# Optimization experiments

Measured on AMD Instinct MI355X. Metric: run time of the kernel, lower is better.

Reference implementation:

```python
import jax, jax.numpy as jnp
import numpy as np

B, L = 16, 512          # samples x tokens-per-sample
S = B * L               # total packed tokens
H, HKV, D = 16, 4, 128  # query heads, kv heads, head_dim
G = H // HKV            # GQA group size
HID = 2048
EPS = 1e-6


def rmsnorm(x, w):
    # Qwen2RMSNorm: fp32 variance, scale by weight
    v = jnp.mean(x.astype(jnp.float32) ** 2, axis=-1, keepdims=True)
    return (x.astype(jnp.float32) * jax.lax.rsqrt(v + EPS)).astype(x.dtype) * w


def rotate_half(x):
    x1, x2 = jnp.split(x, 2, axis=-1)
    return jnp.concatenate([-x2, x1], axis=-1)


def setup_inputs() -> dict:
    key = jax.random.key(0)
    ks = jax.random.split(key, 24)
    f = lambda k, shp, s=0.02: (jax.random.normal(k, shp, dtype=jnp.float32) * s)
    inp = {
        'packed_sequence_und': f(ks[0], (S // 2, HID), 1.0),
        'packed_sequence_gen': f(ks[1], (S // 2, HID), 1.0),
        # und tokens on even slots, gen on odd slots -> irregular scatter
        'packed_und_token_indexes': jnp.arange(0, S, 2, dtype=jnp.int32),
        'packed_gen_token_indexes': jnp.arange(1, S, 2, dtype=jnp.int32),
        # und-path projections (q/k/v have bias, o does not)
        'q_w': f(ks[2], (H * D, HID)), 'q_b': f(ks[3], (H * D,)),
        'k_w': f(ks[4], (HKV * D, HID)), 'k_b': f(ks[5], (HKV * D,)),
        'v_w': f(ks[6], (HKV * D, HID)), 'v_b': f(ks[7], (HKV * D,)),
        'o_w': f(ks[8], (HID, H * D)),
        # gen-path (moe_gen) projections
        'q_w_g': f(ks[9], (H * D, HID)), 'q_b_g': f(ks[10], (H * D,)),
        'k_w_g': f(ks[11], (HKV * D, HID)), 'k_b_g': f(ks[12], (HKV * D,)),
        'v_w_g': f(ks[13], (HKV * D, HID)), 'v_b_g': f(ks[14], (HKV * D,)),
        'o_w_g': f(ks[15], (HID, H * D)),
        # qk-norm weights
        'qn_w': jnp.ones((D,), jnp.float32), 'kn_w': jnp.ones((D,), jnp.float32),
        'qn_w_g': jnp.ones((D,), jnp.float32), 'kn_w_g': jnp.ones((D,), jnp.float32),
    }
    # RoPE cos/sin for packed positions (position resets per sample)
    pos = jnp.tile(jnp.arange(L, dtype=jnp.float32), B)            # [S]
    inv_freq = 1.0 / (1e6 ** (jnp.arange(0, D, 2, dtype=jnp.float32) / D))
    freqs = pos[:, None] * inv_freq[None, :]                       # [S, D/2]
    emb = jnp.concatenate([freqs, freqs], axis=-1)                 # [S, D]
    inp['packed_cos'] = jnp.cos(emb)
    inp['packed_sin'] = jnp.sin(emb)
    return inp


def reference(packed_sequence_und, packed_sequence_gen, packed_cos, packed_sin,
              packed_und_token_indexes, packed_gen_token_indexes,
              q_w, q_b, k_w, k_b, v_w, v_b, o_w,
              q_w_g, q_b_g, k_w_g, k_b_g, v_w_g, v_b_g, o_w_g,
              qn_w, kn_w, qn_w_g, kn_w_g):
    ui, gi = packed_und_token_indexes, packed_gen_token_indexes
    # dual-path QKV projection + index scatter into shared packed buffers
    q = jnp.zeros((S, H * D), jnp.float32)
    q = q.at[ui].set(packed_sequence_und @ q_w.T + q_b)
    q = q.at[gi].set(packed_sequence_gen @ q_w_g.T + q_b_g)
    k = jnp.zeros((S, HKV * D), jnp.float32)
    k = k.at[ui].set(packed_sequence_und @ k_w.T + k_b)
    k = k.at[gi].set(packed_sequence_gen @ k_w_g.T + k_b_g)
    v = jnp.zeros((S, HKV * D), jnp.float32)
    v = v.at[ui].set(packed_sequence_und @ v_w.T + v_b)
    v = v.at[gi].set(packed_sequence_gen @ v_w_g.T + v_b_g)

    q = q.reshape(S, H, D)
    k = k.reshape(S, HKV, D)
    v = v.reshape(S, HKV, D)

    # per-stream QK RMSNorm, scattered back
    q = jnp.zeros_like(q).at[ui].set(rmsnorm(q[ui], qn_w)).at[gi].set(rmsnorm(q[gi], qn_w_g))
    k = jnp.zeros_like(k).at[ui].set(rmsnorm(k[ui], kn_w)).at[gi].set(rmsnorm(k[gi], kn_w_g))

    # RoPE (unsqueeze_dim=1)
    cos, sin = packed_cos[:, None, :], packed_sin[:, None, :]
    q = q * cos + rotate_half(q) * sin
    k = k * cos + rotate_half(k) * sin

    # block-diagonal causal attention over packed samples (GQA)
    qb_ = q.reshape(B, L, HKV, G, D)
    kb_ = k.reshape(B, L, HKV, D)
    vb_ = v.reshape(B, L, HKV, D)
    scale = 1.0 / np.sqrt(D)
    scores = jnp.einsum('bqhgd,bkhd->bhgqk', qb_, kb_) * scale   # [B,HKV,G,L,L]
    causal = jnp.tril(jnp.ones((L, L), bool))
    scores = jnp.where(causal, scores, -jnp.inf)
    probs = jax.nn.softmax(scores, axis=-1)
    out = jnp.einsum('bhgqk,bkhd->bqhgd', probs, vb_)            # [B,L,HKV,G,D]
    out = out.reshape(S, H * D)

    out_und = out[ui] @ o_w.T
    out_gen = out[gi] @ o_w_g.T
    return (out_und, out_gen)
```

## Files before the change

kernel.cpp:

```cpp
#include <hip/hip_runtime.h>

typedef __bf16 bf16;
typedef __bf16 bf16x8 __attribute__((ext_vector_type(8)));
typedef float  f32x4  __attribute__((ext_vector_type(4)));

#define HALF   4096
#define S_TOT  8192
#define HID    2048
#define NH     16
#define NKV    4
#define DH     128
#define LSEQ   512

typedef const __attribute__((address_space(1))) void* as1_cvp;
typedef __attribute__((address_space(3))) void* as3_vp;

__device__ __forceinline__ void gl2lds16(const void* g, void* l) {
    __builtin_amdgcn_global_load_lds((as1_cvp)g, (as3_vp)l, 16, 0, 0);
}

__global__ void k_convert(const float* __restrict__ src, bf16* __restrict__ dst, int n4) {
    int i = blockIdx.x * 256 + threadIdx.x;
    if (i >= n4) return;
    float4 v = ((const float4*)src)[i];
    union { bf16 b[4]; ushort4 u; } t;
    t.b[0] = (bf16)v.x; t.b[1] = (bf16)v.y; t.b[2] = (bf16)v.z; t.b[3] = (bf16)v.w;
    ((ushort4*)dst)[i] = t.u;
}

__global__ void k_invtyp(const int* __restrict__ ui, const int* __restrict__ gi,
                         int* __restrict__ it) {
    int t = blockIdx.x * 256 + threadIdx.x;
    if (t < HALF) { it[ui[t]] = t << 1; it[gi[t]] = (t << 1) | 1; }
}

__global__ __launch_bounds__(256) void k_gemm_qkv(
    const bf16* __restrict__ Xu, const bf16* __restrict__ Xg,
    const bf16* __restrict__ Wu, const bf16* __restrict__ Wg,
    const float* __restrict__ qbu, const float* __restrict__ kbu, const float* __restrict__ vbu,
    const float* __restrict__ qbg, const float* __restrict__ kbg, const float* __restrict__ vbg,
    const int* __restrict__ ui, const int* __restrict__ gi,
    bf16* __restrict__ qo, bf16* __restrict__ ko, bf16* __restrict__ vo)
{
    const int gen = blockIdx.z;
    const bf16* X = gen ? Xg : Xu;
    const bf16* W = gen ? Wg : Wu;
    const float* qb = gen ? qbg : qbu;
    const float* kb = gen ? kbg : kbu;
    const float* vb = gen ? vbg : vbu;
    const int* idx = gen ? gi : ui;

    __shared__ __align__(16) bf16 sA[128*32];
    __shared__ __align__(16) bf16 sB[128*32];

    const int tid = threadIdx.x;
    const int wave = tid >> 6, lane = tid & 63;
    const int lm = lane & 15, kq = lane >> 4;
    const int wm = wave >> 1, wn = wave & 1;
    const int m0 = blockIdx.y * 128, n0 = blockIdx.x * 128;

    f32x4 acc[4][4] = {};

    for (int k0 = 0; k0 < HID; k0 += 32) {
        __syncthreads();
        #pragma unroll
        for (int i = 0; i < 2; ++i) {
            const int g = i*4 + wave;
            const int c = g*64 + lane;
            const int row = c >> 2, col = c & 3;
            gl2lds16(X + (size_t)(m0+row)*HID + k0 + col*8, (char*)sA + (size_t)g*1024);
            gl2lds16(W + (size_t)(n0+row)*HID + k0 + col*8, (char*)sB + (size_t)g*1024);
        }
        __syncthreads();
        bf16x8 a[4], b[4];
        #pragma unroll
        for (int i = 0; i < 4; ++i) a[i] = *(const bf16x8*)&sA[(wm*64 + i*16 + lm)*32 + kq*8];
        #pragma unroll
        for (int j = 0; j < 4; ++j) b[j] = *(const bf16x8*)&sB[(wn*64 + j*16 + lm)*32 + kq*8];
        #pragma unroll
        for (int i = 0; i < 4; ++i)
            #pragma unroll
            for (int j = 0; j < 4; ++j)
                acc[i][j] = __builtin_amdgcn_mfma_f32_16x16x32_bf16(a[i], b[j], acc[i][j], 0, 0, 0);
    }

    #pragma unroll
    for (int i = 0; i < 4; ++i) {
        int srow[4];
        #pragma unroll
        for (int r = 0; r < 4; ++r) srow[r] = idx[m0 + wm*64 + i*16 + kq*4 + r];
        #pragma unroll
        for (int j = 0; j < 4; ++j) {
            const int o = n0 + wn*64 + j*16 + lm;
            bf16* dst; float bias; int off0, ld;
            if (o < 2048)      { dst = qo; ld = 2048; off0 = o;        bias = qb[o]; }
            else if (o < 2560) { dst = ko; ld = 512;  off0 = o - 2048; bias = kb[o-2048]; }
            else               { dst = vo; ld = 512;  off0 = o - 2560; bias = vb[o-2560]; }
            #pragma unroll
            for (int r = 0; r < 4; ++r)
                dst[(size_t)srow[r]*ld + off0] = (bf16)(acc[i][j][r] + bias);
        }
    }
}

__global__ __launch_bounds__(256) void k_norm_rope(
    bf16* __restrict__ qbuf, bf16* __restrict__ kbuf,
    const float* __restrict__ cosb, const float* __restrict__ sinb,
    const int* __restrict__ invtyp,
    const float* __restrict__ qnu, const float* __restrict__ qng,
    const float* __restrict__ knu, const float* __restrict__ kng)
{
    const int row = blockIdx.x * 4 + (threadIdx.x >> 6);
    const int lane = threadIdx.x & 63;
    const int s = row / (NH + NKV), hh = row % (NH + NKV);
    const int isg = invtyp[s] & 1;
    bf16* ptr; const float* w;
    if (hh < NH) { ptr = qbuf + (size_t)s*HID + hh*DH;           w = isg ? qng : qnu; }
    else         { ptr = kbuf + (size_t)s*(NKV*DH) + (hh-NH)*DH; w = isg ? kng : knu; }

    const unsigned u = *(const unsigned*)((const unsigned short*)ptr + 2*lane);
    const float f0 = __uint_as_float(u << 16);
    const float f1 = __uint_as_float(u & 0xffff0000u);
    float ss = f0*f0 + f1*f1;
    #pragma unroll
    for (int m = 32; m; m >>= 1) ss += __shfl_xor(ss, m, 64);
    const float r = rsqrtf(ss * (1.0f/128.0f) + 1e-6f);
    const float2 wv = *(const float2*)(w + 2*lane);
    const float xn0 = f0 * r * wv.x;
    const float xn1 = f1 * r * wv.y;
    const float po0 = __shfl_xor(xn0, 32, 64);
    const float po1 = __shfl_xor(xn1, 32, 64);
    const float2 c2 = *(const float2*)(cosb + (size_t)s*DH + 2*lane);
    const float2 s2 = *(const float2*)(sinb + (size_t)s*DH + 2*lane);
    const float sg = (lane < 32) ? -1.0f : 1.0f;
    const float o0 = xn0 * c2.x + sg * po0 * s2.x;
    const float o1 = xn1 * c2.y + sg * po1 * s2.y;
    union { unsigned short us[2]; unsigned u; } t;
    bf16 b0 = (bf16)o0, b1 = (bf16)o1;
    t.us[0] = *(unsigned short*)&b0; t.us[1] = *(unsigned short*)&b1;
    *(unsigned*)((unsigned short*)ptr + 2*lane) = t.u;
}

__global__ __launch_bounds__(256) void k_vtrans(const bf16* __restrict__ v, bf16* __restrict__ vt)
{
    __shared__ __align__(16) bf16 sT[64 * 132];
    const int kvh = blockIdx.y;
    const int s0 = blockIdx.x * 64;
    const int b = s0 >> 9;
    const int pos0 = s0 & 511;
    const int tid = threadIdx.x;

    #pragma unroll
    for (int i = 0; i < 4; ++i) {
        const int c = i*256 + tid;
        const int rowi = c >> 4, col8 = c & 15;
        const uint4 d = *(const uint4*)(v + (size_t)(s0 + rowi)*(NKV*DH) + kvh*DH + col8*8);
        uint2* lp = (uint2*)&sT[rowi*132 + col8*8];
        lp[0] = make_uint2(d.x, d.y);
        lp[1] = make_uint2(d.z, d.w);
    }
    __syncthreads();
    const int dd = tid >> 1, half = tid & 1;
    __align__(16) bf16 tmp[32];
    #pragma unroll
    for (int p = 0; p < 32; ++p) tmp[p] = sT[(half*32 + p)*132 + dd];
    bf16* dst = vt + ((size_t)(b*NKV + kvh)*DH + dd)*LSEQ + pos0 + half*32;
    #pragma unroll
    for (int q = 0; q < 8; ++q) ((ushort4*)dst)[q] = ((ushort4*)tmp)[q];
}

__global__ __launch_bounds__(256) void k_attn(
    const bf16* __restrict__ qbuf, const bf16* __restrict__ kbuf,
    const bf16* __restrict__ vt, const int* __restrict__ invtyp,
    bf16* __restrict__ aop_u, bf16* __restrict__ aop_g)
{
    __shared__ __align__(16) bf16 sQ[64*128];
    __shared__ __align__(16) bf16 sK[64*128];
    __shared__ __align__(16) bf16 sV[128*64];
    __shared__ __align__(16) bf16 sP[4][16*72];

    const int qt = 7 - blockIdx.x;
    const int h = blockIdx.y, b = blockIdx.z;
    const int kvh = h >> 2;
    const int tid = threadIdx.x, wave = tid >> 6, lane = tid & 63;
    const int lm = lane & 15, kq = lane >> 4;
    const int q0 = qt * 64;

    {
        const bf16* qp = qbuf + ((size_t)(b*LSEQ + q0))*HID + h*DH;
        #pragma unroll
        for (int i = 0; i < 4; ++i) {
            const int g = i*4 + wave;
            const int ch = g*64 + lane;
            const int row = ch >> 4, cp = ch & 15;
            const int c = (cp & 8) | ((cp ^ row) & 7);
            gl2lds16(qp + (size_t)row*HID + c*8, (char*)sQ + (size_t)g*1024);
        }
    }

    f32x4 accO[8] = {};
    float mrow[4], lrow[4];
    #pragma unroll
    for (int r = 0; r < 4; ++r) { mrow[r] = -1e30f; lrow[r] = 0.f; }

    const float scale = 0.08838834764831845f;
    bf16* const sPw = &sP[wave][0];

    for (int kt = 0; kt <= qt; ++kt) {
        __syncthreads();
        {
            const bf16* kp = kbuf + ((size_t)(b*LSEQ + kt*64))*(NKV*DH) + kvh*DH;
            const bf16* vp = vt + ((size_t)(b*NKV + kvh)*DH)*LSEQ + kt*64;
            #pragma unroll
            for (int i = 0; i < 4; ++i) {
                const int g = i*4 + wave;
                const int ch = g*64 + lane;
                { const int row = ch >> 4, cp = ch & 15;
                  const int c = (cp & 8) | ((cp ^ row) & 7);
                  gl2lds16(kp + (size_t)row*(NKV*DH) + c*8, (char*)sK + (size_t)g*1024); }
                { const int d = ch >> 3, cp = ch & 7;
                  const int c = (cp ^ d) & 7;
                  gl2lds16(vp + (size_t)d*LSEQ + c*8, (char*)sV + (size_t)g*1024); }
            }
        }
        __syncthreads();

        f32x4 s4[4] = {};
        #pragma unroll
        for (int ks = 0; ks < 4; ++ks) {
            const int cq = ks*4 + kq;
            const int cs = (cq & 8) | ((cq ^ lm) & 7);
            bf16x8 a = *(const bf16x8*)&sQ[(wave*16 + lm)*128 + cs*8];
            #pragma unroll
            for (int nt = 0; nt < 4; ++nt) {
                bf16x8 bk = *(const bf16x8*)&sK[(nt*16 + lm)*128 + cs*8];
                s4[nt] = __builtin_amdgcn_mfma_f32_16x16x32_bf16(a, bk, s4[nt], 0, 0, 0);
            }
        }

        const bool diag = (kt == qt);
        #pragma unroll
        for (int r = 0; r < 4; ++r) {
            const int rloc = wave*16 + kq*4 + r;
            float v0 = s4[0][r], v1 = s4[1][r], v2 = s4[2][r], v3 = s4[3][r];
            if (diag) {
                if (lm      > rloc) v0 = -1e30f;
                if (lm + 16 > rloc) v1 = -1e30f;
                if (lm + 32 > rloc) v2 = -1e30f;
                if (lm + 48 > rloc) v3 = -1e30f;
            }
            float m = fmaxf(fmaxf(v0, v1), fmaxf(v2, v3));
            m = fmaxf(m, __shfl_xor(m, 1, 64));
            m = fmaxf(m, __shfl_xor(m, 2, 64));
            m = fmaxf(m, __shfl_xor(m, 4, 64));
            m = fmaxf(m, __shfl_xor(m, 8, 64));
            const float mnew = fmaxf(mrow[r], m);
            const float p0 = __expf((v0 - mnew) * scale);
            const float p1 = __expf((v1 - mnew) * scale);
            const float p2 = __expf((v2 - mnew) * scale);
            const float p3 = __expf((v3 - mnew) * scale);
            float rs = (p0 + p1) + (p2 + p3);
            rs += __shfl_xor(rs, 1, 64);
            rs += __shfl_xor(rs, 2, 64);
            rs += __shfl_xor(rs, 4, 64);
            rs += __shfl_xor(rs, 8, 64);
            const float alpha = __expf((mrow[r] - mnew) * scale);
            lrow[r] = lrow[r] * alpha + rs;
            mrow[r] = mnew;
            #pragma unroll
            for (int dt = 0; dt < 8; ++dt) accO[dt][r] *= alpha;
            const int prow = (kq*4 + r) * 72;
            sPw[prow + lm]      = (bf16)p0;
            sPw[prow + 16 + lm] = (bf16)p1;
            sPw[prow + 32 + lm] = (bf16)p2;
            sPw[prow + 48 + lm] = (bf16)p3;
        }

        #pragma unroll
        for (int pc = 0; pc < 2; ++pc) {
            bf16x8 ap = *(const bf16x8*)&sPw[lm*72 + pc*32 + kq*8];
            #pragma unroll
            for (int dt = 0; dt < 8; ++dt) {
                const int cv = (pc*4 + kq);
                const int cs = (cv ^ lm) & 7;
                bf16x8 bv = *(const bf16x8*)&sV[(dt*16 + lm)*64 + cs*8];
                accO[dt] = __builtin_amdgcn_mfma_f32_16x16x32_bf16(ap, bv, accO[dt], 0, 0, 0);
            }
        }
    }

    #pragma unroll
    for (int r = 0; r < 4; ++r) {
        const int srow = b*LSEQ + q0 + wave*16 + kq*4 + r;
        const int code = invtyp[srow];
        bf16* dst = (code & 1) ? aop_g : aop_u;
        const size_t off = (size_t)(code >> 1)*HID + h*DH;
        const float inv_l = 1.0f / lrow[r];
        #pragma unroll
        for (int dt = 0; dt < 8; ++dt)
            dst[off + dt*16 + lm] = (bf16)(accO[dt][r] * inv_l);
    }
}

__global__ __launch_bounds__(256) void k_gemm_out(
    const bf16* __restrict__ Au, const bf16* __restrict__ Ag,
    const bf16* __restrict__ Wu, const bf16* __restrict__ Wg,
    float* __restrict__ out)
{
    const int gen = blockIdx.z;
    const bf16* A = gen ? Ag : Au;
    const bf16* W = gen ? Wg : Wu;
    float* O = out + (size_t)gen * HALF * HID;

    __shared__ __align__(16) bf16 sA[128*32];
    __shared__ __align__(16) bf16 sB[128*32];

    const int tid = threadIdx.x;
    const int wave = tid >> 6, lane = tid & 63;
    const int lm = lane & 15, kq = lane >> 4;
    const int wm = wave >> 1, wn = wave & 1;
    const int m0 = blockIdx.y * 128, n0 = blockIdx.x * 128;

    f32x4 acc[4][4] = {};

    for (int k0 = 0; k0 < HID; k0 += 32) {
        __syncthreads();
        #pragma unroll
        for (int i = 0; i < 2; ++i) {
            const int g = i*4 + wave;
            const int c = g*64 + lane;
            const int row = c >> 2, col = c & 3;
            gl2lds16(A + (size_t)(m0+row)*HID + k0 + col*8, (char*)sA + (size_t)g*1024);
            gl2lds16(W + (size_t)(n0+row)*HID + k0 + col*8, (char*)sB + (size_t)g*1024);
        }
        __syncthreads();
        bf16x8 a[4], b[4];
        #pragma unroll
        for (int i = 0; i < 4; ++i) a[i] = *(const bf16x8*)&sA[(wm*64 + i*16 + lm)*32 + kq*8];
        #pragma unroll
        for (int j = 0; j < 4; ++j) b[j] = *(const bf16x8*)&sB[(wn*64 + j*16 + lm)*32 + kq*8];
        #pragma unroll
        for (int i = 0; i < 4; ++i)
            #pragma unroll
            for (int j = 0; j < 4; ++j)
                acc[i][j] = __builtin_amdgcn_mfma_f32_16x16x32_bf16(a[i], b[j], acc[i][j], 0, 0, 0);
    }

    #pragma unroll
    for (int i = 0; i < 4; ++i)
        #pragma unroll
        for (int j = 0; j < 4; ++j)
            #pragma unroll
            for (int r = 0; r < 4; ++r)
                O[(size_t)(m0 + wm*64 + i*16 + kq*4 + r)*HID + (n0 + wn*64 + j*16 + lm)] = acc[i][j][r];
}

extern "C" void kernel_launch(void* const* d_in, const int* in_sizes, int n_in,
                              void* d_out, int out_size, void* d_ws, size_t ws_size,
                              hipStream_t stream)
{
    (void)in_sizes; (void)n_in; (void)out_size; (void)ws_size;
    const float* x_u  = (const float*)d_in[0];
    const float* x_g  = (const float*)d_in[1];
    const int*   ui   = (const int*)d_in[2];
    const int*   gi   = (const int*)d_in[3];
    const float* q_w  = (const float*)d_in[4];
    const float* q_b  = (const float*)d_in[5];
    const float* k_w  = (const float*)d_in[6];
    const float* k_b  = (const float*)d_in[7];
    const float* v_w  = (const float*)d_in[8];
    const float* v_b  = (const float*)d_in[9];
    const float* o_w  = (const float*)d_in[10];
    const float* q_wg = (const float*)d_in[11];
    const float* q_bg = (const float*)d_in[12];
    const float* k_wg = (const float*)d_in[13];
    const float* k_bg = (const float*)d_in[14];
    const float* v_wg = (const float*)d_in[15];
    const float* v_bg = (const float*)d_in[16];
    const float* o_wg = (const float*)d_in[17];
    const float* qn_u = (const float*)d_in[18];
    const float* kn_u = (const float*)d_in[19];
    const float* qn_g = (const float*)d_in[20];
    const float* kn_g = (const float*)d_in[21];
    const float* cosb = (const float*)d_in[22];
    const float* sinb = (const float*)d_in[23];

    char* w = (char*)d_ws;
    auto alloc = [&](size_t bytes) { char* p = w; w += (bytes + 255) & ~(size_t)255; return p; };
    bf16* xb_u   = (bf16*)alloc((size_t)HALF*HID*2);
    bf16* xb_g   = (bf16*)alloc((size_t)HALF*HID*2);
    bf16* wqkv_u = (bf16*)alloc((size_t)3072*HID*2);
    bf16* wqkv_g = (bf16*)alloc((size_t)3072*HID*2);
    bf16* qbuf   = (bf16*)alloc((size_t)S_TOT*HID*2);
    bf16* kbuf   = (bf16*)alloc((size_t)S_TOT*NKV*DH*2);
    bf16* vbuf   = (bf16*)alloc((size_t)S_TOT*NKV*DH*2);
    bf16* vtb    = (bf16*)alloc((size_t)S_TOT*NKV*DH*2);
    int*  invtyp = (int*)alloc((size_t)S_TOT*4);
    bf16* aop_u = xb_u;
    bf16* aop_g = xb_g;
    bf16* wo_u  = wqkv_u;
    bf16* wo_g  = wqkv_g;

    auto cvt = [&](const float* s, bf16* d, size_t n) {
        int n4 = (int)(n / 4);
        k_convert<<<(n4 + 255)/256, 256, 0, stream>>>(s, d, n4);
    };

    cvt(x_u, xb_u, (size_t)HALF*HID);
    cvt(x_g, xb_g, (size_t)HALF*HID);
    cvt(q_w,  wqkv_u,               (size_t)2048*HID);
    cvt(k_w,  wqkv_u + 2048*HID,    (size_t)512*HID);
    cvt(v_w,  wqkv_u + 2560*HID,    (size_t)512*HID);
    cvt(q_wg, wqkv_g,               (size_t)2048*HID);
    cvt(k_wg, wqkv_g + 2048*HID,    (size_t)512*HID);
    cvt(v_wg, wqkv_g + 2560*HID,    (size_t)512*HID);
    k_invtyp<<<16, 256, 0, stream>>>(ui, gi, invtyp);

    k_gemm_qkv<<<dim3(24, 32, 2), 256, 0, stream>>>(
        xb_u, xb_g, wqkv_u, wqkv_g,
        q_b, k_b, v_b, q_bg, k_bg, v_bg,
        ui, gi, qbuf, kbuf, vbuf);

    k_norm_rope<<<(S_TOT*(NH+NKV))/4, 256, 0, stream>>>(
        qbuf, kbuf, cosb, sinb, invtyp, qn_u, qn_g, kn_u, kn_g);

    k_vtrans<<<dim3(S_TOT/64, NKV), 256, 0, stream>>>(vbuf, vtb);

    k_attn<<<dim3(LSEQ/64, NH, 16), 256, 0, stream>>>(
        qbuf, kbuf, vtb, invtyp, aop_u, aop_g);

    cvt(o_w,  wo_u, (size_t)HID*HID);
    cvt(o_wg, wo_g, (size_t)HID*HID);

    k_gemm_out<<<dim3(16, 32, 2), 256, 0, stream>>>(
        aop_u, aop_g, wo_u, wo_g, (float*)d_out);
}
```

Baseline: 607.4 us.

## Batch all conversions into one kernel and fold softmax scale into Q

Merges the ten fp32-to-bf16 conversion launches into a single multi-segment kernel, with separate workspace buffers for the output-projection weights so they can be converted up front. Q is pre-scaled by softmax scale times log2(e) in the norm/RoPE kernel so attention can use exp2 without a per-element multiply. Q fragments are now held in registers and the Q shared-memory buffer is reused for P, which cuts LDS footprint. The per-tile row-sum shuffle reduction is deferred to the end of the attention loop. Trade-offs are a larger workspace and slightly different bf16 rounding of the scaled Q.

```diff
diff --git a/kernel.cpp b/kernel.cpp
--- a/kernel.cpp
+++ b/kernel.cpp
@@ -19,13 +19,26 @@
     __builtin_amdgcn_global_load_lds((as1_cvp)g, (as3_vp)l, 16, 0, 0);
 }
 
-__global__ void k_convert(const float* __restrict__ src, bf16* __restrict__ dst, int n4) {
+struct CvtArgs {
+    const float* src[10];
+    bf16*        dst[10];
+    int          n4[10];
+};
+__global__ __launch_bounds__(256) void k_convert_multi(CvtArgs a, int total4) {
     int i = blockIdx.x * 256 + threadIdx.x;
-    if (i >= n4) return;
-    float4 v = ((const float4*)src)[i];
-    union { bf16 b[4]; ushort4 u; } t;
-    t.b[0] = (bf16)v.x; t.b[1] = (bf16)v.y; t.b[2] = (bf16)v.z; t.b[3] = (bf16)v.w;
-    ((ushort4*)dst)[i] = t.u;
+    if (i >= total4) return;
+    int off = i;
+    #pragma unroll
+    for (int s = 0; s < 10; ++s) {
+        if (off < a.n4[s]) {
+            float4 v = ((const float4*)a.src[s])[off];
+            union { bf16 b[4]; ushort4 u; } t;
+            t.b[0] = (bf16)v.x; t.b[1] = (bf16)v.y; t.b[2] = (bf16)v.z; t.b[3] = (bf16)v.w;
+            ((ushort4*)a.dst[s])[off] = t.u;
+            return;
+        }
+        off -= a.n4[s];
+    }
 }
 
 __global__ void k_invtyp(const int* __restrict__ ui, const int* __restrict__ gi,
@@ -114,9 +127,11 @@
     const int lane = threadIdx.x & 63;
     const int s = row / (NH + NKV), hh = row % (NH + NKV);
     const int isg = invtyp[s] & 1;
-    bf16* ptr; const float* w;
-    if (hh < NH) { ptr = qbuf + (size_t)s*HID + hh*DH;           w = isg ? qng : qnu; }
-    else         { ptr = kbuf + (size_t)s*(NKV*DH) + (hh-NH)*DH; w = isg ? kng : knu; }
+    bf16* ptr; const float* w; float qs;
+    if (hh < NH) { ptr = qbuf + (size_t)s*HID + hh*DH;           w = isg ? qng : qnu;
+                   qs = 0.08838834764831845f * 1.4426950408889634f; }
+    else         { ptr = kbuf + (size_t)s*(NKV*DH) + (hh-NH)*DH; w = isg ? kng : knu;
+                   qs = 1.0f; }
 
     const unsigned u = *(const unsigned*)((const unsigned short*)ptr + 2*lane);
     const float f0 = __uint_as_float(u << 16);
@@ -133,8 +148,8 @@
     const float2 c2 = *(const float2*)(cosb + (size_t)s*DH + 2*lane);
     const float2 s2 = *(const float2*)(sinb + (size_t)s*DH + 2*lane);
     const float sg = (lane < 32) ? -1.0f : 1.0f;
-    const float o0 = xn0 * c2.x + sg * po0 * s2.x;
-    const float o1 = xn1 * c2.y + sg * po1 * s2.y;
+    const float o0 = (xn0 * c2.x + sg * po0 * s2.x) * qs;
+    const float o1 = (xn1 * c2.y + sg * po1 * s2.y) * qs;
     union { unsigned short us[2]; unsigned u; } t;
     bf16 b0 = (bf16)o0, b1 = (bf16)o1;
     t.us[0] = *(unsigned short*)&b0; t.us[1] = *(unsigned short*)&b1;
@@ -174,10 +189,9 @@
     const bf16* __restrict__ vt, const int* __restrict__ invtyp,
     bf16* __restrict__ aop_u, bf16* __restrict__ aop_g)
 {
-    __shared__ __align__(16) bf16 sQ[64*128];
     __shared__ __align__(16) bf16 sK[64*128];
     __shared__ __align__(16) bf16 sV[128*64];
-    __shared__ __align__(16) bf16 sP[4][16*72];
+    __shared__ __align__(16) bf16 sQP[64*128];
 
     const int qt = 7 - blockIdx.x;
     const int h = blockIdx.y, b = blockIdx.z;
@@ -194,17 +208,24 @@
             const int ch = g*64 + lane;
             const int row = ch >> 4, cp = ch & 15;
             const int c = (cp & 8) | ((cp ^ row) & 7);
-            gl2lds16(qp + (size_t)row*HID + c*8, (char*)sQ + (size_t)g*1024);
-        }
+            gl2lds16(qp + (size_t)row*HID + c*8, (char*)sQP + (size_t)g*1024);
+        }
+    }
+    __syncthreads();
+    bf16x8 qfrag[4];
+    #pragma unroll
+    for (int ks = 0; ks < 4; ++ks) {
+        const int cq = ks*4 + kq;
+        const int cs = (cq & 8) | ((cq ^ lm) & 7);
+        qfrag[ks] = *(const bf16x8*)&sQP[(wave*16 + lm)*128 + cs*8];
     }
 
     f32x4 accO[8] = {};
-    float mrow[4], lrow[4];
-    #pragma unroll
-    for (int r = 0; r < 4; ++r) { mrow[r] = -1e30f; lrow[r] = 0.f; }
-
-    const float scale = 0.08838834764831845f;
-    bf16* const sPw = &sP[wave][0];
+    float mrow[4], lpart[4];
+    #pragma unroll
+    for (int r = 0; r < 4; ++r) { mrow[r] = -1e30f; lpart[r] = 0.f; }
+
+    bf16* const sPw = &sQP[wave * (16*72)];
 
     for (int kt = 0; kt <= qt; ++kt) {
         __syncthreads();
@@ -230,11 +251,10 @@
         for (int ks = 0; ks < 4; ++ks) {
             const int cq = ks*4 + kq;
             const int cs = (cq & 8) | ((cq ^ lm) & 7);
-            bf16x8 a = *(const bf16x8*)&sQ[(wave*16 + lm)*128 + cs*8];
             #pragma unroll
             for (int nt = 0; nt < 4; ++nt) {
                 bf16x8 bk = *(const bf16x8*)&sK[(nt*16 + lm)*128 + cs*8];
-                s4[nt] = __builtin_amdgcn_mfma_f32_16x16x32_bf16(a, bk, s4[nt], 0, 0, 0);
+                s4[nt] = __builtin_amdgcn_mfma_f32_16x16x32_bf16(qfrag[ks], bk, s4[nt], 0, 0, 0);
             }
         }
 
@@ -255,17 +275,12 @@
             m = fmaxf(m, __shfl_xor(m, 4, 64));
             m = fmaxf(m, __shfl_xor(m, 8, 64));
             const float mnew = fmaxf(mrow[r], m);
-            const float p0 = __expf((v0 - mnew) * scale);
-            const float p1 = __expf((v1 - mnew) * scale);
-            const float p2 = __expf((v2 - mnew) * scale);
-            const float p3 = __expf((v3 - mnew) * scale);
-            float rs = (p0 + p1) + (p2 + p3);
-            rs += __shfl_xor(rs, 1, 64);
-            rs += __shfl_xor(rs, 2, 64);
-            rs += __shfl_xor(rs, 4, 64);
-            rs += __shfl_xor(rs, 8, 64);
-            const float alpha = __expf((mrow[r] - mnew) * scale);
-            lrow[r] = lrow[r] * alpha + rs;
+            const float p0 = exp2f(v0 - mnew);
+            const float p1 = exp2f(v1 - mnew);
+            const float p2 = exp2f(v2 - mnew);
+            const float p3 = exp2f(v3 - mnew);
+            const float alpha = exp2f(mrow[r] - mnew);
+            lpart[r] = lpart[r] * alpha + ((p0 + p1) + (p2 + p3));
             mrow[r] = mnew;
             #pragma unroll
             for (int dt = 0; dt < 8; ++dt) accO[dt][r] *= alpha;
@@ -291,11 +306,16 @@
 
     #pragma unroll
     for (int r = 0; r < 4; ++r) {
+        float l = lpart[r];
+        l += __shfl_xor(l, 1, 64);
+        l += __shfl_xor(l, 2, 64);
+        l += __shfl_xor(l, 4, 64);
+        l += __shfl_xor(l, 8, 64);
         const int srow = b*LSEQ + q0 + wave*16 + kq*4 + r;
         const int code = invtyp[srow];
         bf16* dst = (code & 1) ? aop_g : aop_u;
         const size_t off = (size_t)(code >> 1)*HID + h*DH;
-        const float inv_l = 1.0f / lrow[r];
+        const float inv_l = 1.0f / l;
         #pragma unroll
         for (int dt = 0; dt < 8; ++dt)
             dst[off + dt*16 + lm] = (bf16)(accO[dt][r] * inv_l);
@@ -391,6 +411,8 @@
     bf16* xb_g   = (bf16*)alloc((size_t)HALF*HID*2);
     bf16* wqkv_u = (bf16*)alloc((size_t)3072*HID*2);
     bf16* wqkv_g = (bf16*)alloc((size_t)3072*HID*2);
+    bf16* wo_u   = (bf16*)alloc((size_t)HID*HID*2);
+    bf16* wo_g   = (bf16*)alloc((size_t)HID*HID*2);
     bf16* qbuf   = (bf16*)alloc((size_t)S_TOT*HID*2);
     bf16* kbuf   = (bf16*)alloc((size_t)S_TOT*NKV*DH*2);
     bf16* vbuf   = (bf16*)alloc((size_t)S_TOT*NKV*DH*2);
@@ -398,22 +420,25 @@
     int*  invtyp = (int*)alloc((size_t)S_TOT*4);
     bf16* aop_u = xb_u;
     bf16* aop_g = xb_g;
-    bf16* wo_u  = wqkv_u;
-    bf16* wo_g  = wqkv_g;
-
-    auto cvt = [&](const float* s, bf16* d, size_t n) {
-        int n4 = (int)(n / 4);
-        k_convert<<<(n4 + 255)/256, 256, 0, stream>>>(s, d, n4);
+
+    CvtArgs ca;
+    int total4 = 0, si = 0;
+    auto seg = [&](const float* s, bf16* d, size_t n) {
+        ca.src[si] = s; ca.dst[si] = d; ca.n4[si] = (int)(n / 4);
+        total4 += (int)(n / 4); ++si;
     };
-
-    cvt(x_u, xb_u, (size_t)HALF*HID);
-    cvt(x_g, xb_g, (size_t)HALF*HID);
-    cvt(q_w,  wqkv_u,               (size_t)2048*HID);
-    cvt(k_w,  wqkv_u + 2048*HID,    (size_t)512*HID);
-    cvt(v_w,  wqkv_u + 2560*HID,    (size_t)512*HID);
-    cvt(q_wg, wqkv_g,               (size_t)2048*HID);
-    cvt(k_wg, wqkv_g + 2048*HID,    (size_t)512*HID);
-    cvt(v_wg, wqkv_g + 2560*HID,    (size_t)512*HID);
+    seg(x_u,  xb_u,                (size_t)HALF*HID);
+    seg(x_g,  xb_g,                (size_t)HALF*HID);
+    seg(q_w,  wqkv_u,              (size_t)2048*HID);
+    seg(k_w,  wqkv_u + 2048*HID,   (size_t)512*HID);
+    seg(v_w,  wqkv_u + 2560*HID,   (size_t)512*HID);
+    seg(q_wg, wqkv_g,              (size_t)2048*HID);
+    seg(k_wg, wqkv_g + 2048*HID,   (size_t)512*HID);
+    seg(v_wg, wqkv_g + 2560*HID,   (size_t)512*HID);
+    seg(o_w,  wo_u,                (size_t)HID*HID);
+    seg(o_wg, wo_g,                (size_t)HID*HID);
+    k_convert_multi<<<(total4 + 255)/256, 256, 0, stream>>>(ca, total4);
+
     k_invtyp<<<16, 256, 0, stream>>>(ui, gi, invtyp);
 
     k_gemm_qkv<<<dim3(24, 32, 2), 256, 0, stream>>>(
@@ -429,9 +454,6 @@
     k_attn<<<dim3(LSEQ/64, NH, 16), 256, 0, stream>>>(
         qbuf, kbuf, vtb, invtyp, aop_u, aop_g);
 
-    cvt(o_w,  wo_u, (size_t)HID*HID);
-    cvt(o_wg, wo_g, (size_t)HID*HID);
-
     k_gemm_out<<<dim3(16, 32, 2), 256, 0, stream>>>(
         aop_u, aop_g, wo_u, wo_g, (float*)d_out);
 }
```

New measurement: 582.8 us. 4.0% less time.
